# Kernel tuning notes

Hardware: AMD Instinct MI355X
Metric: run time of the kernel (lower is better)

Reference implementation:

```python
import jax, jax.numpy as jnp
import numpy as np

EPS = 1e-12

def _prelu(x, a):
    return jnp.where(x >= 0, x, a * x)

def _l2norm(x):
    n = jnp.sqrt(jnp.sum(x * x, axis=1, keepdims=True))
    return x / jnp.maximum(n, EPS)

def setup_inputs() -> dict:
    key = jax.random.key(0)
    ks = jax.random.split(key, 8)
    N, E, F_IN, F_OUT = 262144, 4194304, 128, 64
    feat = jax.random.normal(ks[0], (N, F_IN), dtype=jnp.float32)
    edge_src = jax.random.randint(ks[1], (E,), 0, N, dtype=jnp.int32)
    edge_dst = jax.random.randint(ks[2], (E,), 0, N, dtype=jnp.int32)
    edge_w = jax.random.uniform(ks[3], (E,), dtype=jnp.float32)
    # Glorot-uniform projection weight, zero biases (reset_parameters)
    lim = float(np.sqrt(6.0 / (F_IN + F_OUT)))
    weight = jax.random.uniform(ks[4], (F_IN, F_OUT), minval=-lim, maxval=lim, dtype=jnp.float32)
    bias = jnp.zeros((F_OUT,), dtype=jnp.float32)
    prelu_a = jnp.full((1,), 0.25, dtype=jnp.float32)
    lim2 = float(np.sqrt(1.0 / F_OUT))  # torch Linear default init range
    w_sub = jax.random.uniform(ks[5], (F_OUT, F_OUT), minval=-lim2, maxval=lim2, dtype=jnp.float32)
    b_sub = jnp.zeros((F_OUT,), dtype=jnp.float32)
    w_gcn = jax.random.uniform(ks[6], (F_OUT, F_OUT), minval=-lim2, maxval=lim2, dtype=jnp.float32)
    b_gcn = jnp.zeros((F_OUT,), dtype=jnp.float32)
    return {"feat": feat, "edge_src": edge_src, "edge_dst": edge_dst, "edge_w": edge_w,
            "weight": weight, "bias": bias, "prelu_a": prelu_a,
            "w_sub": w_sub, "b_sub": b_sub, "w_gcn": w_gcn, "b_gcn": b_gcn}

def reference(feat, edge_src, edge_dst, edge_w, weight, bias, prelu_a,
              w_sub, b_sub, w_gcn, b_gcn):
    N = feat.shape[0]
    G = N // 4  # 4 nodes per subgraph, anchors at stride 4
    # anchor rows extracted, then zeroed in the feature matrix (in-place in torch)
    anchor_embs = feat[::4, :]
    feat_z = feat.at[::4, :].set(0.0)
    anchor_out = _prelu(anchor_embs @ weight + bias, prelu_a)
    # GraphConv(norm='none', weight=False, bias=False) with edge weights:
    # h[dst] = sum_e w_e * (feat_z @ W)[src_e]
    in_feat = feat_z @ weight                      # [N, F_OUT]
    msgs = in_feat[edge_src] * edge_w[:, None]     # [E, F_OUT]
    h = jax.ops.segment_sum(msgs, edge_dst, num_segments=N)
    h = _prelu(h + bias, prelu_a)
    # AvgPooling per graph (each graph has exactly 4 nodes)
    seg = jnp.arange(N, dtype=jnp.int32) // 4
    subgraph_pool_emb = jax.ops.segment_sum(h, seg, num_segments=G) / 4.0
    gcn_emb = h[::4, :]
    subgraph_pool_emb = subgraph_pool_emb @ w_sub.T + b_sub
    gcn_emb = gcn_emb @ w_gcn.T + b_gcn
    return (_l2norm(subgraph_pool_emb), _l2norm(anchor_out), _l2norm(gcn_emb))
```

## Files before the change

### kernel.cpp

```cpp
#include <hip/hip_runtime.h>
#include <hip/hip_fp16.h>

#define EPSN 1e-12f
#define NBC  256
#define RBF  1024
#define CHK  8192
#define NWGMAX 1024
#define PU   4
#define WQS  16384.0f

typedef _Float16 half8_t __attribute__((ext_vector_type(8)));
typedef float    f32x4  __attribute__((ext_vector_type(4)));

__device__ __forceinline__ float rdlane(float v, int k) {
    return __int_as_float(__builtin_amdgcn_readlane(__float_as_int(v), k));
}
__device__ __forceinline__ float preluf(float x, float a) {
    return x >= 0.0f ? x : a * x;
}

__device__ __forceinline__ void transform_body(
    const float* __restrict__ feat, const float* __restrict__ weight,
    const float* __restrict__ bias, const float* __restrict__ prelu_a,
    __half* __restrict__ in_feat, float* __restrict__ out_anchor,
    int N, int wid, int totalWaves)
{
    const int lane = threadIdx.x & 63;
    const int r    = lane & 15;
    const int g    = lane >> 4;
    const int nt4  = N >> 4;

    half8_t bfr[4][4];
    #pragma unroll
    for (int nt = 0; nt < 4; ++nt)
        #pragma unroll
        for (int kq = 0; kq < 4; ++kq)
            #pragma unroll
            for (int e = 0; e < 8; ++e)
                bfr[nt][kq][e] =
                    (_Float16)weight[(kq * 32 + g * 8 + e) * 64 + nt * 16 + r];

    float bj[4];
    #pragma unroll
    for (int nt = 0; nt < 4; ++nt) bj[nt] = bias[nt * 16 + r];
    const float a = prelu_a[0];

    for (int t = wid; t < nt4; t += totalWaves) {
        const int rb = t << 4;

        f32x4 acc[4];
        #pragma unroll
        for (int nt = 0; nt < 4; ++nt) acc[nt] = (f32x4){0.f, 0.f, 0.f, 0.f};

        const float* fr = feat + (size_t)(rb + r) * 128 + g * 8;
        #pragma unroll
        for (int kq = 0; kq < 4; ++kq) {
            const float4 f0 = *(const float4*)(fr + kq * 32);
            const float4 f1 = *(const float4*)(fr + kq * 32 + 4);
            half8_t af;
            af[0] = (_Float16)f0.x; af[1] = (_Float16)f0.y;
            af[2] = (_Float16)f0.z; af[3] = (_Float16)f0.w;
            af[4] = (_Float16)f1.x; af[5] = (_Float16)f1.y;
            af[6] = (_Float16)f1.z; af[7] = (_Float16)f1.w;
            #pragma unroll
            for (int nt = 0; nt < 4; ++nt)
                acc[nt] = __builtin_amdgcn_mfma_f32_16x16x32_f16(
                    af, bfr[nt][kq], acc[nt], 0, 0, 0);
        }

        const int row0 = rb + g * 4;
        float ss = 0.0f, y[4];
        #pragma unroll
        for (int nt = 0; nt < 4; ++nt) {
            y[nt] = preluf(acc[nt][0] + bj[nt], a);
            ss = fmaf(y[nt], y[nt], ss);
        }
        ss += __shfl_xor(ss, 1, 16);
        ss += __shfl_xor(ss, 2, 16);
        ss += __shfl_xor(ss, 4, 16);
        ss += __shfl_xor(ss, 8, 16);
        const float inv = 1.0f / fmaxf(sqrtf(ss), EPSN);
        #pragma unroll
        for (int nt = 0; nt < 4; ++nt)
            out_anchor[(size_t)(row0 >> 2) * 64 + nt * 16 + r] = y[nt] * inv;
        #pragma unroll
        for (int nt = 0; nt < 4; ++nt)
            in_feat[(size_t)row0 * 64 + nt * 16 + r] = __float2half(0.0f);
        #pragma unroll
        for (int reg = 1; reg < 4; ++reg)
            #pragma unroll
            for (int nt = 0; nt < 4; ++nt)
                in_feat[(size_t)(row0 + reg) * 64 + nt * 16 + r] =
                    __float2half(acc[nt][reg]);
    }
}

__global__ __launch_bounds__(256) void k_tc(
    const float* __restrict__ feat, const float* __restrict__ weight,
    const float* __restrict__ bias, const float* __restrict__ prelu_a,
    __half* __restrict__ in_feat, float* __restrict__ out_anchor, int N,
    int nbT, int twT,
    const int* __restrict__ esrc, const int* __restrict__ edst, int E,
    unsigned* __restrict__ C)
{
    __shared__ unsigned hist[NBC];
    const int t = threadIdx.x;
    if ((int)blockIdx.x < nbT) {
        const int wid = (int)((blockIdx.x * (size_t)blockDim.x + t) >> 6);
        transform_body(feat, weight, bias, prelu_a, in_feat, out_anchor,
                       N, wid, twT);
        return;
    }
    const int blk = (int)blockIdx.x - nbT;
    hist[t] = 0;
    __syncthreads();
    const int base = blk * CHK;
    for (int r = 0; r < CHK / (16 * 256); ++r) {
        int d[16];
        #pragma unroll
        for (int i = 0; i < 16; ++i) {
            const int idx = base + (r * 16 + i) * 256 + t;
            d[i] = -1;
            if (idx < E) {
                const int s = esrc[idx];
                if ((s & 3) != 0) d[i] = edst[idx];
            }
        }
        #pragma unroll
        for (int i = 0; i < 16; ++i)
            if (d[i] >= 0) atomicAdd(&hist[((unsigned)d[i]) >> 10], 1u);
    }
    __syncthreads();
    C[(size_t)blk * NBC + t] = hist[t];
}

__global__ __launch_bounds__(256) void s_scanA(
    unsigned* __restrict__ C, unsigned* __restrict__ T, int nwg)
{
    __shared__ unsigned ssum[256];
    const int i = blockIdx.x;
    const int t = threadIdx.x;
    const int PER = (nwg + 255) / 256;
    unsigned vals[4];
    unsigned run = 0;
    for (int p = 0; p < PER; ++p) {
        const int blk = t * PER + p;
        const unsigned v = (blk < nwg) ? C[(size_t)blk * NBC + i] : 0u;
        vals[p] = run;
        run += v;
    }
    ssum[t] = run;
    __syncthreads();
    for (int off = 1; off < 256; off <<= 1) {
        unsigned x = (t >= off) ? ssum[t - off] : 0u;
        __syncthreads();
        ssum[t] += x;
        __syncthreads();
    }
    const unsigned texcl = ssum[t] - run;
    for (int p = 0; p < PER; ++p) {
        const int blk = t * PER + p;
        if (blk < nwg) C[(size_t)blk * NBC + i] = texcl + vals[p];
    }
    if (t == 255) T[i] = ssum[255];
}

__global__ __launch_bounds__(256) void s_scatter4(
    const int* __restrict__ esrc, const int* __restrict__ edst,
    const float* __restrict__ ew, int E,
    const unsigned* __restrict__ C, const unsigned* __restrict__ T, int nwg,
    uint2* __restrict__ recs)
{
    __shared__ uint2    buf[CHK];
    __shared__ unsigned cur[NBC];
    __shared__ unsigned cb [NBC];
    __shared__ unsigned ssum[256];
    const int blk = blockIdx.x;
    const int t   = threadIdx.x;

    const unsigned Tt = T[t];
    ssum[t] = Tt;
    __syncthreads();
    for (int off = 1; off < 256; off <<= 1) {
        unsigned x = (t >= off) ? ssum[t - off] : 0u;
        __syncthreads();
        ssum[t] += x;
        __syncthreads();
    }
    const unsigned basepl = ssum[t] - Tt;
    __syncthreads();

    const unsigned own = C[(size_t)blk * NBC + t];
    const unsigned nxt = (blk + 1 < nwg) ? C[(size_t)(blk + 1) * NBC + t] : Tt;
    const unsigned myc = nxt - own;
    ssum[t] = myc;
    __syncthreads();
    for (int off = 1; off < 256; off <<= 1) {
        unsigned x = (t >= off) ? ssum[t - off] : 0u;
        __syncthreads();
        ssum[t] += x;
        __syncthreads();
    }
    const unsigned excl = ssum[t] - myc;
    cur[t] = excl;
    cb[t]  = basepl + own - excl;
    __syncthreads();
    const unsigned cnt = ssum[255];

    const int base = blk * CHK;
    for (int r = 0; r < CHK / (16 * 256); ++r) {
        int s[16], d[16]; float wv[16];
        #pragma unroll
        for (int i = 0; i < 16; ++i) {
            const int idx = base + (r * 16 + i) * 256 + t;
            const bool ok = (idx < E);
            s[i]  = ok ? esrc[idx] : 0;
            d[i]  = ok ? edst[idx] : 0;
            wv[i] = ok ? ew[idx]   : 0.0f;
            if (!ok || (s[i] & 3) == 0) d[i] = -1;
        }
        #pragma unroll
        for (int i = 0; i < 16; ++i) {
            if (d[i] >= 0) {
                const unsigned slot = atomicAdd(&cur[((unsigned)d[i]) >> 10], 1u);
                const unsigned wq =
                    min((unsigned)(wv[i] * WQS + 0.5f), 16383u);
                buf[slot] = make_uint2(((unsigned)s[i]) | (wq << 18),
                                       (unsigned)d[i]);
            }
        }
    }
    __syncthreads();
    for (unsigned i = t; i < cnt; i += 256) {
        const uint2 rr = buf[i];
        recs[cb[rr.y >> 10] + i] = rr;
    }
}

__global__ __launch_bounds__(256) void s_sortfine(
    const uint2* __restrict__ recs, const unsigned* __restrict__ T,
    unsigned* __restrict__ recf, unsigned* __restrict__ rs, int N)
{
    __shared__ unsigned hist[RBF], cur[RBF], ssum[256];
    const int t = threadIdx.x;
    const int b = blockIdx.x;

    const unsigned Tt = T[t];
    ssum[t] = Tt;
    __syncthreads();
    for (int off = 1; off < 256; off <<= 1) {
        unsigned x = (t >= off) ? ssum[t - off] : 0u;
        __syncthreads();
        ssum[t] += x;
        __syncthreads();
    }
    const unsigned start = (b == 0) ? 0u : ssum[b - 1];
    const unsigned end   = ssum[b];
    if (b == NBC - 1 && t == 0) rs[N] = ssum[NBC - 1];
    __syncthreads();

    #pragma unroll
    for (int p = 0; p < 4; ++p) hist[t * 4 + p] = 0;
    __syncthreads();
    for (unsigned i = start + t; i < end; i += 256)
        atomicAdd(&hist[recs[i].y & (RBF - 1u)], 1u);
    __syncthreads();
    unsigned vals[4], run = 0;
    #pragma unroll
    for (int p = 0; p < 4; ++p) { vals[p] = run; run += hist[t * 4 + p]; }
    ssum[t] = run;
    __syncthreads();
    for (int off = 1; off < 256; off <<= 1) {
        unsigned x = (t >= off) ? ssum[t - off] : 0u;
        __syncthreads();
        ssum[t] += x;
        __syncthreads();
    }
    const unsigned texcl = ssum[t] - run;
    #pragma unroll
    for (int p = 0; p < 4; ++p) {
        const int i = t * 4 + p;
        const unsigned e = start + texcl + vals[p];
        cur[i] = e;
        rs[b * RBF + i] = e;
    }
    __syncthreads();
    for (unsigned i = start + t; i < end; i += 256) {
        const uint2 r = recs[i];
        const unsigned slot = atomicAdd(&cur[r.y & (RBF - 1u)], 1u);
        recf[slot] = r.x;
    }
}

__global__ __launch_bounds__(256) void s_accum5(
    const __half* __restrict__ in_feat, const unsigned* __restrict__ recf,
    const unsigned* __restrict__ rs, float* __restrict__ h,
    int NROWS, int totalWaves)
{
    const char* ifb  = (const char*)in_feat;
    const int   lane = threadIdx.x & 63;
    const int   l32  = lane & 31;
    const int   hsel = lane >> 5;
    const unsigned colb = (unsigned)l32 * 4u;
    const int wid = (int)((blockIdx.x * (size_t)blockDim.x + threadIdx.x) >> 6);

    for (int row = wid; row < NROWS; row += totalWaves) {
        const unsigned s = rs[row], e = rs[row + 1];
        float acc0 = 0.0f, acc1 = 0.0f;
        for (unsigned done = s; done < e; done += 64u) {
            const int c = (int)min(64u, e - done);
            unsigned rcd = 0u;
            if (lane < c) rcd = recf[done + lane];
            const int pairs = (c + 1) >> 1;
            for (int p0 = 0; p0 < pairs; p0 += PU) {
                unsigned px[PU];
                __half2  hh[PU];
                float    wj[PU];
                #pragma unroll
                for (int pp = 0; pp < PU; ++pp) {
                    const int jv = (p0 + pp) * 2 + hsel;
                    px[pp] = (unsigned)__shfl((int)rcd, jv, 64);
                }
                #pragma unroll
                for (int pp = 0; pp < PU; ++pp) {
                    const unsigned voff =
                        ((px[pp] & 0x3FFFFu) << 7) + colb;
                    hh[pp] = *(const __half2*)(ifb + (size_t)voff);
                    wj[pp] = (float)(px[pp] >> 18);
                }
                #pragma unroll
                for (int pp = 0; pp < PU; ++pp) {
                    acc0 = fmaf(__half2float(__low2half(hh[pp])),  wj[pp], acc0);
                    acc1 = fmaf(__half2float(__high2half(hh[pp])), wj[pp], acc1);
                }
            }
        }
        acc0 += __shfl_xor(acc0, 32, 64);
        acc1 += __shfl_xor(acc1, 32, 64);
        if (hsel == 0) {
            float2 o;
            o.x = acc0 * (1.0f / WQS);
            o.y = acc1 * (1.0f / WQS);
            *(float2*)(h + ((size_t)row << 6) + 2 * l32) = o;
        }
    }
}

__global__ __launch_bounds__(256) void k_transform2(
    const float* __restrict__ feat, const float* __restrict__ weight,
    const float* __restrict__ bias, const float* __restrict__ prelu_a,
    __half* __restrict__ in_feat, float* __restrict__ out_anchor,
    int N, int totalWaves)
{
    const int lane  = threadIdx.x & 63;
    const int wid   = (int)((blockIdx.x * (size_t)blockDim.x + threadIdx.x) >> 6);
    const int tiles = (N + 63) >> 6;

    for (int tile = wid; tile < tiles; tile += totalWaves) {
        const int row = tile * 64 + lane;
        if (row >= N) continue;

        float acc[64];
        #pragma unroll
        for (int j = 0; j < 64; ++j) acc[j] = 0.0f;

        const float4* fp = (const float4*)(feat + (size_t)row * 128);
        #pragma unroll 4
        for (int kc = 0; kc < 32; ++kc) {
            const float4 f = fp[kc];
            const float fs[4] = {f.x, f.y, f.z, f.w};
            #pragma unroll
            for (int kk = 0; kk < 4; ++kk) {
                const float fv = fs[kk];
                const float* wr = weight + (kc * 4 + kk) * 64;
                #pragma unroll
                for (int j = 0; j < 64; ++j)
                    acc[j] = fmaf(fv, wr[j], acc[j]);
            }
        }

        if ((row & 3) == 0) {
            const float a = prelu_a[0];
            float ss = 0.0f;
            #pragma unroll
            for (int j = 0; j < 64; ++j) {
                acc[j] = preluf(acc[j] + bias[j], a);
                ss = fmaf(acc[j], acc[j], ss);
            }
            const float inv = 1.0f / fmaxf(sqrtf(ss), EPSN);
            float* ap = out_anchor + (size_t)(row >> 2) * 64;
            #pragma unroll
            for (int j = 0; j < 64; ++j) ap[j] = acc[j] * inv;
            #pragma unroll
            for (int j = 0; j < 64; ++j)
                in_feat[(size_t)row * 64 + j] = __float2half(0.0f);
        } else {
            #pragma unroll
            for (int j = 0; j < 64; ++j)
                in_feat[(size_t)row * 64 + j] = __float2half(acc[j]);
        }
    }
}

#define K2_U 8
__global__ __launch_bounds__(256) void k_edges(
    const __half* __restrict__ in_feat, const int* __restrict__ esrc,
    const int* __restrict__ edst, const float* __restrict__ ew,
    float* __restrict__ h, int E, int totalWaves)
{
    const int lane = threadIdx.x & 63;
    int wid = (int)((blockIdx.x * (size_t)blockDim.x + threadIdx.x) >> 6);
    wid = __builtin_amdgcn_readfirstlane(wid);
    const int chunk = (E + totalWaves - 1) / totalWaves;
    int e0 = wid * chunk;
    int e1 = min(e0 + chunk, E);
    for (int base = e0; base < e1; base += K2_U) {
        const int nb = min(K2_U, e1 - base);
        int s[K2_U], d[K2_U]; float w[K2_U];
        #pragma unroll
        for (int j = 0; j < K2_U; ++j) {
            int idx = base + ((j < nb) ? j : 0);
            s[j] = esrc[idx]; d[j] = edst[idx]; w[j] = ew[idx];
        }
        float v[K2_U];
        #pragma unroll
        for (int j = 0; j < K2_U; ++j)
            v[j] = __half2float(in_feat[((size_t)s[j] << 6) + lane]);
        #pragma unroll
        for (int j = 0; j < K2_U; ++j)
            if (j < nb) atomicAdd(h + ((size_t)d[j] << 6) + lane, v[j] * w[j]);
    }
}

__global__ __launch_bounds__(256) void k_finalize(
    const float* __restrict__ h, const float* __restrict__ bias,
    const float* __restrict__ prelu_a,
    const float* __restrict__ w_sub, const float* __restrict__ b_sub,
    const float* __restrict__ w_gcn, const float* __restrict__ b_gcn,
    float* __restrict__ out_sub, float* __restrict__ out_gcn,
    int G, int totalWaves)
{
    const int lane = threadIdx.x & 63;
    const int wid = (int)((blockIdx.x * (size_t)blockDim.x + threadIdx.x) >> 6);

    float wsreg[64], wgreg[64];
    #pragma unroll
    for (int k = 0; k < 64; ++k) wsreg[k] = w_sub[lane * 64 + k];
    #pragma unroll
    for (int k = 0; k < 64; ++k) wgreg[k] = w_gcn[lane * 64 + k];
    const float bj  = bias[lane];
    const float bsj = b_sub[lane];
    const float bgj = b_gcn[lane];
    const float a   = prelu_a[0];

    for (int g = wid; g < G; g += totalWaves) {
        const float* hp = h + (size_t)g * 256;
        float p0 = preluf(hp[lane]       + bj, a);
        float p1 = preluf(hp[64  + lane] + bj, a);
        float p2 = preluf(hp[128 + lane] + bj, a);
        float p3 = preluf(hp[192 + lane] + bj, a);
        float pool = (p0 + p1 + p2 + p3) * 0.25f;
        float gcn  = p0;

        float as = bsj, ag = bgj;
        #pragma unroll
        for (int k = 0; k < 64; ++k) {
            as = fmaf(rdlane(pool, k), wsreg[k], as);
            ag = fmaf(rdlane(gcn,  k), wgreg[k], ag);
        }
        float ss = as * as, sg = ag * ag;
        #pragma unroll
        for (int off = 32; off >= 1; off >>= 1) {
            ss += __shfl_xor(ss, off, 64);
            sg += __shfl_xor(sg, off, 64);
        }
        out_sub[(size_t)g * 64 + lane] = as / fmaxf(sqrtf(ss), EPSN);
        out_gcn[(size_t)g * 64 + lane] = ag / fmaxf(sqrtf(sg), EPSN);
    }
}

extern "C" void kernel_launch(void* const* d_in, const int* in_sizes, int n_in,
                              void* d_out, int out_size, void* d_ws, size_t ws_size,
                              hipStream_t stream)
{
    const float* feat    = (const float*)d_in[0];
    const int*   esrc    = (const int*)  d_in[1];
    const int*   edst    = (const int*)  d_in[2];
    const float* ew      = (const float*)d_in[3];
    const float* weight  = (const float*)d_in[4];
    const float* bias    = (const float*)d_in[5];
    const float* prelu_a = (const float*)d_in[6];
    const float* w_sub   = (const float*)d_in[7];
    const float* b_sub   = (const float*)d_in[8];
    const float* w_gcn   = (const float*)d_in[9];
    const float* b_gcn   = (const float*)d_in[10];

    const int N = in_sizes[0] / 128;
    const int E = in_sizes[1];
    const int G = N / 4;
    const int nwg = (E + CHK - 1) / CHK;

    char* wsb = (char*)d_ws;
    const size_t AH    = (size_t)N * 64 * 2;
    const size_t A     = (size_t)N * 64 * 4;
    const size_t offRf = AH + A;
    const size_t offC  = offRf + (size_t)E * 4;
    const size_t offT  = offC  + (size_t)nwg * NBC * 4;
    const size_t offRs = offT  + (size_t)NBC * 4;
    const size_t ws_need = offRs + (size_t)(N + 1) * 4;

    __half*   in_feat = (__half*)wsb;
    float*    h       = (float*)(wsb + AH);
    uint2*    recs    = (uint2*)(wsb + AH);
    unsigned* recf    = (unsigned*)(wsb + offRf);
    unsigned* C       = (unsigned*)(wsb + offC);
    unsigned* T       = (unsigned*)(wsb + offT);
    unsigned* rs      = (unsigned*)(wsb + offRs);

    float* out        = (float*)d_out;
    float* out_sub    = out;
    float* out_anchor = out + (size_t)G * 64;
    float* out_gcn    = out + (size_t)2 * G * 64;

    const bool sorted_path =
        (N == NBC * RBF) && (nwg <= NWGMAX) && ((size_t)E * 8 <= A) &&
        (ws_size >= ws_need);

    if (sorted_path) {
        {
            const int nbT = 1024, twT = nbT * 4;
            k_tc<<<nbT + nwg, 256, 0, stream>>>(feat, weight, bias, prelu_a,
                                                in_feat, out_anchor, N, nbT, twT,
                                                esrc, edst, E, C);
        }
        s_scanA   <<<NBC, 256, 0, stream>>>(C, T, nwg);
        s_scatter4<<<nwg, 256, 0, stream>>>(esrc, edst, ew, E, C, T, nwg, recs);
        s_sortfine<<<NBC, 256, 0, stream>>>(recs, T, recf, rs, N);
        {
            const int blocks = 2048, tw = blocks * 4;
            s_accum5<<<blocks, 256, 0, stream>>>(in_feat, recf, rs, h, N, tw);
        }
        {
            const int blocks = 4096, tw = blocks * 4;
            k_finalize<<<blocks, 256, 0, stream>>>(h, bias, prelu_a, w_sub, b_sub,
                                                   w_gcn, b_gcn, out_sub, out_gcn, G, tw);
        }
    } else if (ws_size >= AH + A) {
        {
            const int blocks = 1024, tw = blocks * 4;
            k_transform2<<<blocks, 256, 0, stream>>>(feat, weight, bias, prelu_a,
                                                     in_feat, out_anchor, N, tw);
        }
        hipMemsetAsync(h, 0, A, stream);
        const int blocks = 2048, tw = blocks * 4;
        k_edges<<<blocks, 256, 0, stream>>>(in_feat, esrc, edst, ew, h, E, tw);
        const int fblocks = 4096, ftw = fblocks * 4;
        k_finalize<<<fblocks, 256, 0, stream>>>(h, bias, prelu_a, w_sub, b_sub,
                                                w_gcn, b_gcn, out_sub, out_gcn, G, ftw);
    }
}
```

Baseline: 481.4 us.

## Widen scatter and fine-sort blocks to 1024 threads, reorder histogram-first launch

The fused transform/histogram kernel now puts the histogram blocks first in the grid and doubles the number of transform blocks. The coarse scatter and fine sort kernels move from 256 to 1024 threads per block. The scatter kernel handles its 8192-edge chunk in a single pass, and the fine sort gives each thread one bin with a 1024-wide scan. The aim is more parallelism and memory-level concurrency in the partitioning stages, and an earlier start for the histogram work. In exchange the scans carry more barrier steps and more threads sit idle in the 256-wide phases.

```diff
diff --git a/kernel.cpp b/kernel.cpp
--- a/kernel.cpp
+++ b/kernel.cpp
@@ -99,19 +99,20 @@
     const float* __restrict__ feat, const float* __restrict__ weight,
     const float* __restrict__ bias, const float* __restrict__ prelu_a,
     __half* __restrict__ in_feat, float* __restrict__ out_anchor, int N,
-    int nbT, int twT,
+    int nwg, int twT,
     const int* __restrict__ esrc, const int* __restrict__ edst, int E,
     unsigned* __restrict__ C)
 {
     __shared__ unsigned hist[NBC];
     const int t = threadIdx.x;
-    if ((int)blockIdx.x < nbT) {
-        const int wid = (int)((blockIdx.x * (size_t)blockDim.x + t) >> 6);
+    if ((int)blockIdx.x >= nwg) {
+        const int tIdx = (int)blockIdx.x - nwg;
+        const int wid  = tIdx * 4 + (t >> 6);
         transform_body(feat, weight, bias, prelu_a, in_feat, out_anchor,
                        N, wid, twT);
         return;
     }
-    const int blk = (int)blockIdx.x - nbT;
+    const int blk = (int)blockIdx.x;
     hist[t] = 0;
     __syncthreads();
     const int base = blk * CHK;
@@ -165,7 +166,7 @@
     if (t == 255) T[i] = ssum[255];
 }
 
-__global__ __launch_bounds__(256) void s_scatter4(
+__global__ __launch_bounds__(1024) void s_scatter4(
     const int* __restrict__ esrc, const int* __restrict__ edst,
     const float* __restrict__ ew, int E,
     const unsigned* __restrict__ C, const unsigned* __restrict__ T, int nwg,
@@ -174,120 +175,119 @@
     __shared__ uint2    buf[CHK];
     __shared__ unsigned cur[NBC];
     __shared__ unsigned cb [NBC];
-    __shared__ unsigned ssum[256];
+    __shared__ unsigned ssum[NBC];
     const int blk = blockIdx.x;
     const int t   = threadIdx.x;
 
-    const unsigned Tt = T[t];
-    ssum[t] = Tt;
-    __syncthreads();
-    for (int off = 1; off < 256; off <<= 1) {
-        unsigned x = (t >= off) ? ssum[t - off] : 0u;
-        __syncthreads();
-        ssum[t] += x;
-        __syncthreads();
-    }
-    const unsigned basepl = ssum[t] - Tt;
-    __syncthreads();
-
-    const unsigned own = C[(size_t)blk * NBC + t];
-    const unsigned nxt = (blk + 1 < nwg) ? C[(size_t)(blk + 1) * NBC + t] : Tt;
+    unsigned Tt = 0, own = 0, nxt = 0;
+    if (t < NBC) {
+        Tt  = T[t];
+        own = C[(size_t)blk * NBC + t];
+        nxt = (blk + 1 < nwg) ? C[(size_t)(blk + 1) * NBC + t] : Tt;
+        ssum[t] = Tt;
+    }
+    __syncthreads();
+    for (int off = 1; off < NBC; off <<= 1) {
+        unsigned x = 0;
+        if (t < NBC && t >= off) x = ssum[t - off];
+        __syncthreads();
+        if (t < NBC) ssum[t] += x;
+        __syncthreads();
+    }
+    const unsigned basepl = (t < NBC) ? (ssum[t] - Tt) : 0u;
+    __syncthreads();
+
     const unsigned myc = nxt - own;
-    ssum[t] = myc;
-    __syncthreads();
-    for (int off = 1; off < 256; off <<= 1) {
-        unsigned x = (t >= off) ? ssum[t - off] : 0u;
-        __syncthreads();
-        ssum[t] += x;
-        __syncthreads();
-    }
-    const unsigned excl = ssum[t] - myc;
-    cur[t] = excl;
-    cb[t]  = basepl + own - excl;
-    __syncthreads();
-    const unsigned cnt = ssum[255];
+    if (t < NBC) ssum[t] = myc;
+    __syncthreads();
+    for (int off = 1; off < NBC; off <<= 1) {
+        unsigned x = 0;
+        if (t < NBC && t >= off) x = ssum[t - off];
+        __syncthreads();
+        if (t < NBC) ssum[t] += x;
+        __syncthreads();
+    }
+    if (t < NBC) {
+        const unsigned excl = ssum[t] - myc;
+        cur[t] = excl;
+        cb[t]  = basepl + own - excl;
+    }
+    __syncthreads();
+    const unsigned cnt = ssum[NBC - 1];
 
     const int base = blk * CHK;
-    for (int r = 0; r < CHK / (16 * 256); ++r) {
-        int s[16], d[16]; float wv[16];
-        #pragma unroll
-        for (int i = 0; i < 16; ++i) {
-            const int idx = base + (r * 16 + i) * 256 + t;
-            const bool ok = (idx < E);
-            s[i]  = ok ? esrc[idx] : 0;
-            d[i]  = ok ? edst[idx] : 0;
-            wv[i] = ok ? ew[idx]   : 0.0f;
-            if (!ok || (s[i] & 3) == 0) d[i] = -1;
-        }
-        #pragma unroll
-        for (int i = 0; i < 16; ++i) {
-            if (d[i] >= 0) {
-                const unsigned slot = atomicAdd(&cur[((unsigned)d[i]) >> 10], 1u);
-                const unsigned wq =
-                    min((unsigned)(wv[i] * WQS + 0.5f), 16383u);
-                buf[slot] = make_uint2(((unsigned)s[i]) | (wq << 18),
-                                       (unsigned)d[i]);
-            }
-        }
-    }
-    __syncthreads();
-    for (unsigned i = t; i < cnt; i += 256) {
+    int s8[8], d8[8]; float w8[8];
+    #pragma unroll
+    for (int i = 0; i < 8; ++i) {
+        const int idx = base + i * 1024 + t;
+        const bool ok = (idx < E);
+        s8[i] = ok ? esrc[idx] : 0;
+        d8[i] = ok ? edst[idx] : 0;
+        w8[i] = ok ? ew[idx]   : 0.0f;
+        if (!ok || (s8[i] & 3) == 0) d8[i] = -1;
+    }
+    #pragma unroll
+    for (int i = 0; i < 8; ++i) {
+        if (d8[i] >= 0) {
+            const unsigned slot = atomicAdd(&cur[((unsigned)d8[i]) >> 10], 1u);
+            const unsigned wq = min((unsigned)(w8[i] * WQS + 0.5f), 16383u);
+            buf[slot] = make_uint2(((unsigned)s8[i]) | (wq << 18),
+                                   (unsigned)d8[i]);
+        }
+    }
+    __syncthreads();
+    for (unsigned i = t; i < cnt; i += 1024) {
         const uint2 rr = buf[i];
         recs[cb[rr.y >> 10] + i] = rr;
     }
 }
 
-__global__ __launch_bounds__(256) void s_sortfine(
+__global__ __launch_bounds__(1024) void s_sortfine(
     const uint2* __restrict__ recs, const unsigned* __restrict__ T,
     unsigned* __restrict__ recf, unsigned* __restrict__ rs, int N)
 {
-    __shared__ unsigned hist[RBF], cur[RBF], ssum[256];
+    __shared__ unsigned hist[RBF];
+    __shared__ unsigned sc[RBF];
+    __shared__ unsigned bs[NBC];
     const int t = threadIdx.x;
     const int b = blockIdx.x;
 
-    const unsigned Tt = T[t];
-    ssum[t] = Tt;
-    __syncthreads();
-    for (int off = 1; off < 256; off <<= 1) {
-        unsigned x = (t >= off) ? ssum[t - off] : 0u;
-        __syncthreads();
-        ssum[t] += x;
-        __syncthreads();
-    }
-    const unsigned start = (b == 0) ? 0u : ssum[b - 1];
-    const unsigned end   = ssum[b];
-    if (b == NBC - 1 && t == 0) rs[N] = ssum[NBC - 1];
-    __syncthreads();
-
-    #pragma unroll
-    for (int p = 0; p < 4; ++p) hist[t * 4 + p] = 0;
-    __syncthreads();
-    for (unsigned i = start + t; i < end; i += 256)
+    const unsigned Tb = T[b];
+    if (t < NBC) bs[t] = T[t];
+    __syncthreads();
+    for (int off = 1; off < NBC; off <<= 1) {
+        unsigned x = 0;
+        if (t < NBC && t >= off) x = bs[t - off];
+        __syncthreads();
+        if (t < NBC) bs[t] += x;
+        __syncthreads();
+    }
+    const unsigned end   = bs[b];
+    const unsigned start = end - Tb;
+    if (b == NBC - 1 && t == 0) rs[N] = bs[NBC - 1];
+    __syncthreads();
+
+    hist[t] = 0;
+    __syncthreads();
+    for (unsigned i = start + t; i < end; i += 1024)
         atomicAdd(&hist[recs[i].y & (RBF - 1u)], 1u);
     __syncthreads();
-    unsigned vals[4], run = 0;
-    #pragma unroll
-    for (int p = 0; p < 4; ++p) { vals[p] = run; run += hist[t * 4 + p]; }
-    ssum[t] = run;
-    __syncthreads();
-    for (int off = 1; off < 256; off <<= 1) {
-        unsigned x = (t >= off) ? ssum[t - off] : 0u;
-        __syncthreads();
-        ssum[t] += x;
-        __syncthreads();
-    }
-    const unsigned texcl = ssum[t] - run;
-    #pragma unroll
-    for (int p = 0; p < 4; ++p) {
-        const int i = t * 4 + p;
-        const unsigned e = start + texcl + vals[p];
-        cur[i] = e;
-        rs[b * RBF + i] = e;
-    }
-    __syncthreads();
-    for (unsigned i = start + t; i < end; i += 256) {
+    const unsigned my = hist[t];
+    sc[t] = my;
+    __syncthreads();
+    for (int off = 1; off < RBF; off <<= 1) {
+        unsigned x = (t >= off) ? sc[t - off] : 0u;
+        __syncthreads();
+        sc[t] += x;
+        __syncthreads();
+    }
+    const unsigned rowstart = start + sc[t] - my;
+    hist[t] = rowstart;
+    rs[b * RBF + t] = rowstart;
+    __syncthreads();
+    for (unsigned i = start + t; i < end; i += 1024) {
         const uint2 r = recs[i];
-        const unsigned slot = atomicAdd(&cur[r.y & (RBF - 1u)], 1u);
+        const unsigned slot = atomicAdd(&hist[r.y & (RBF - 1u)], 1u);
         recf[slot] = r.x;
     }
 }
@@ -528,14 +528,14 @@
 
     if (sorted_path) {
         {
-            const int nbT = 1024, twT = nbT * 4;
-            k_tc<<<nbT + nwg, 256, 0, stream>>>(feat, weight, bias, prelu_a,
-                                                in_feat, out_anchor, N, nbT, twT,
+            const int nbT = 2048, twT = nbT * 4;
+            k_tc<<<nwg + nbT, 256, 0, stream>>>(feat, weight, bias, prelu_a,
+                                                in_feat, out_anchor, N, nwg, twT,
                                                 esrc, edst, E, C);
         }
         s_scanA   <<<NBC, 256, 0, stream>>>(C, T, nwg);
-        s_scatter4<<<nwg, 256, 0, stream>>>(esrc, edst, ew, E, C, T, nwg, recs);
-        s_sortfine<<<NBC, 256, 0, stream>>>(recs, T, recf, rs, N);
+        s_scatter4<<<nwg, 1024, 0, stream>>>(esrc, edst, ew, E, C, T, nwg, recs);
+        s_sortfine<<<NBC, 1024, 0, stream>>>(recs, T, recf, rs, N);
         {
             const int blocks = 2048, tw = blocks * 4;
             s_accum5<<<blocks, 256, 0, stream>>>(in_feat, recf, rs, h, N, tw);
```

Result: faster. 462.1 us (-4.0%).
